# Optimization experiments

Hardware: AMD Instinct MI355X
Metric: run time of the kernel (lower is better)

## Reference

```python
import math
import jax, jax.numpy as jnp
import numpy as np

B, C, H, W = 2, 256, 128, 128
C8 = C // 8
MAX_TOKENS = 4096
S = int(math.isqrt(MAX_TOKENS))  # 64; H,W divisible by S -> exact 2x2 mean pool


def setup_inputs() -> dict:
    key = jax.random.key(0)
    ks = jax.random.split(key, 8)
    sc = 1.0 / math.sqrt(C)
    return {
        "x": jax.random.normal(ks[0], (B, C, H, W), dtype=jnp.float32),
        "Wq": jax.random.normal(ks[1], (C8, C), dtype=jnp.float32) * sc,
        "bq": jax.random.normal(ks[2], (C8,), dtype=jnp.float32) * 0.01,
        "Wk": jax.random.normal(ks[3], (C8, C), dtype=jnp.float32) * sc,
        "bk": jax.random.normal(ks[4], (C8,), dtype=jnp.float32) * 0.01,
        "Wv": jax.random.normal(ks[5], (C, C), dtype=jnp.float32) * sc,
        "bv": jax.random.normal(ks[6], (C,), dtype=jnp.float32) * 0.01,
        # torch inits gamma to 0; use small nonzero so the attention path is exercised
        "gamma": jax.random.normal(ks[7], (1,), dtype=jnp.float32) * 0.1,
    }


def _pool_to_s(t):
    # adaptive_avg_pool2d to (S,S); exact since H%S==0, W%S==0
    b, ch, h, w = t.shape
    return t.reshape(b, ch, S, h // S, S, w // S).mean(axis=(3, 5))


def reference(x, Wq, bq, Wk, bk, Wv, bv, gamma):
    b, c, h, w = x.shape
    # 1x1 convs as channel contractions
    q = jnp.einsum('bchw,oc->bohw', x, Wq) + bq[None, :, None, None]   # (b,c8,h,w)
    k = jnp.einsum('bchw,oc->bohw', x, Wk) + bk[None, :, None, None]   # (b,c8,h,w)
    v = jnp.einsum('bchw,oc->bohw', x, Wv) + bv[None, :, None, None]   # (b,c,h,w)

    q = q.reshape(b, C8, h * w).transpose(0, 2, 1)                      # (b, hw, c8)
    if h * w > MAX_TOKENS:
        k = _pool_to_s(k)
        v = _pool_to_s(v)
    k = k.reshape(b, C8, -1)                                            # (b, c8, s2)
    v = v.reshape(b, c, -1)                                             # (b, c, s2)

    attn = jnp.einsum('btc,bcs->bts', q, k) / math.sqrt(k.shape[1])     # (b, hw, s2)
    attn = jax.nn.softmax(attn, axis=-1)
    out = jnp.einsum('bcs,bts->bct', v, attn).reshape(b, c, h, w)
    return gamma[0] * out + x
```

## Files before the change

### kernel.cpp

```cpp
#include <hip/hip_runtime.h>

typedef unsigned short u16;
typedef unsigned int u32;
typedef unsigned long long u64;
typedef float f32x4 __attribute__((ext_vector_type(4)));
typedef __bf16 bf16x8 __attribute__((ext_vector_type(8)));

__device__ __forceinline__ u16 f2bf(float f) {
  unsigned u = __float_as_uint(f);
  unsigned r = u + 0x7fffu + ((u >> 16) & 1u);
  return (u16)(r >> 16);
}
__device__ __forceinline__ u32 cvt_pk_bf16(float lo, float hi) {
  u32 r;
  asm("v_cvt_pk_bf16_f32 %0, %1, %2" : "=v"(r) : "v"(lo), "v"(hi));
  return r;
}
__device__ __forceinline__ float exp2_hw(float x) {
  float r;
  asm("v_exp_f32 %0, %1" : "=v"(r) : "v"(x));
  return r;
}
__device__ __forceinline__ bf16x8 f32x8_to_bf16x8(float4 a, float4 b) {
  union { u32 u[4]; bf16x8 v; } t;
  t.u[0] = cvt_pk_bf16(a.x, a.y);
  t.u[1] = cvt_pk_bf16(a.z, a.w);
  t.u[2] = cvt_pk_bf16(b.x, b.y);
  t.u[3] = cvt_pk_bf16(b.z, b.w);
  return t.v;
}
__device__ __forceinline__ void gload_lds16(const void* g, u16* l) {
  __builtin_amdgcn_global_load_lds(
      (const __attribute__((address_space(1))) unsigned int*)g,
      (__attribute__((address_space(3))) unsigned int*)l, 16, 0, 0);
}

#define QSCALE 0.25513936f

__global__ __launch_bounds__(256) void proj_kernel(
    const float* __restrict__ x, const float* __restrict__ Wq, const float* __restrict__ bq,
    const float* __restrict__ Wk, const float* __restrict__ bk, const float* __restrict__ Wv,
    const float* __restrict__ bv, u16* __restrict__ Qb, u16* __restrict__ Kt,
    u16* __restrict__ Vb) {
  __shared__ __align__(16) u16 smem[24576];
  const int tid = threadIdx.x;
  const int lane = tid & 63, w = tid >> 6;
  const int l15 = lane & 15, l4 = lane >> 4;
  const int bi = blockIdx.x;
  const f32x4 zero = {0.f, 0.f, 0.f, 0.f};

  if (bi >= 256) {
    u16* xt = smem;
    u16* wq = smem + 16384;
    const int j = bi - 256;
    const int b = j >> 8, tb = j & 255;
    const float* xp = x + (size_t)b * 256 * 16384 + tb * 64;

    for (int i = tid; i < 4096; i += 256) {
      int oc = i >> 7, c0 = (i & 127) * 2;
      float2 f = *reinterpret_cast<const float2*>(Wq + oc * 256 + c0);
      u32 pk = cvt_pk_bf16(f.x * QSCALE, f.y * QSCALE);
      *reinterpret_cast<u32*>((char*)wq + oc * 512 + (((c0 >> 3) ^ (oc & 7)) * 16) +
                              (c0 & 7) * 2) = pk;
    }
#pragma unroll
    for (int rr = 0; rr < 4; ++rr) {
      int c = rr * 64 + (tid >> 2);
      int tch = (tid & 3) * 16;
      const float* src = xp + (size_t)c * 16384 + tch;
#pragma unroll
      for (int u = 0; u < 4; ++u) {
        float4 f = *reinterpret_cast<const float4*>(src + u * 4);
        int t = tch + u * 4;
        *reinterpret_cast<u16*>((char*)xt + (t + 0) * 512 + (((c >> 3) ^ ((t + 0) & 7)) * 16) + (c & 7) * 2) = f2bf(f.x);
        *reinterpret_cast<u16*>((char*)xt + (t + 1) * 512 + (((c >> 3) ^ ((t + 1) & 7)) * 16) + (c & 7) * 2) = f2bf(f.y);
        *reinterpret_cast<u16*>((char*)xt + (t + 2) * 512 + (((c >> 3) ^ ((t + 2) & 7)) * 16) + (c & 7) * 2) = f2bf(f.z);
        *reinterpret_cast<u16*>((char*)xt + (t + 3) * 512 + (((c >> 3) ^ ((t + 3) & 7)) * 16) + (c & 7) * 2) = f2bf(f.w);
      }
    }
    __syncthreads();

    f32x4 acc[2] = {zero, zero};
    const int tl = w * 16 + l15;
#pragma unroll
    for (int k = 0; k < 8; ++k) {
      bf16x8 bf = *reinterpret_cast<const bf16x8*>((char*)xt + tl * 512 +
                                                   (((k * 4 + l4) ^ (tl & 7)) * 16));
#pragma unroll
      for (int m = 0; m < 2; ++m) {
        int oc = m * 16 + l15;
        bf16x8 af = *reinterpret_cast<const bf16x8*>((char*)wq + oc * 512 +
                                                     (((k * 4 + l4) ^ (oc & 7)) * 16));
        acc[m] = __builtin_amdgcn_mfma_f32_16x16x32_bf16(af, bf, acc[m], 0, 0, 0);
      }
    }
    const int t = tb * 64 + tl;
#pragma unroll
    for (int m = 0; m < 2; ++m) {
      int oc0 = m * 16 + l4 * 4;
      u32 p0 = cvt_pk_bf16(acc[m][0] + bq[oc0] * QSCALE, acc[m][1] + bq[oc0 + 1] * QSCALE);
      u32 p1 = cvt_pk_bf16(acc[m][2] + bq[oc0 + 2] * QSCALE, acc[m][3] + bq[oc0 + 3] * QSCALE);
      u16* dst = Qb + ((size_t)b * 16384 + t) * 32 + oc0;
      *reinterpret_cast<u32*>(dst) = p0;
      *reinterpret_cast<u32*>(dst + 2) = p1;
    }
  } else {
    u16* xs = smem;
    const int b = bi >> 7, r2 = bi & 127;
    const int sy = r2 >> 1, z = r2 & 1;
    const int mb = z * 8;
    const float* xb = x + (size_t)b * 256 * 16384;

#pragma unroll
    for (int rr = 0; rr < 4; ++rr) {
      int c = rr * 64 + (tid >> 2);
      int f4base = (tid & 3) * 8;
      const float* r0 = xb + (size_t)c * 16384 + (size_t)sy * 256;
#pragma unroll
      for (int u = 0; u < 8; ++u) {
        int jj = f4base + u;
        float4 a = *reinterpret_cast<const float4*>(r0 + jj * 4);
        float4 d = *reinterpret_cast<const float4*>(r0 + 128 + jj * 4);
        float p0 = (a.x + a.y + d.x + d.y) * 0.25f;
        float p1 = (a.z + a.w + d.z + d.w) * 0.25f;
        int s0 = jj * 2;
        *reinterpret_cast<u16*>((char*)xs + (s0 + 0) * 512 + (((c >> 3) ^ ((s0 + 0) & 7)) * 16) + (c & 7) * 2) = f2bf(p0);
        *reinterpret_cast<u16*>((char*)xs + (s0 + 1) * 512 + (((c >> 3) ^ ((s0 + 1) & 7)) * 16) + (c & 7) * 2) = f2bf(p1);
      }
    }
    __syncthreads();

    f32x4 acc[10];
#pragma unroll
    for (int m = 0; m < 10; ++m) acc[m] = zero;
    const int sl = w * 16 + l15;
#pragma unroll
    for (int k = 0; k < 8; ++k) {
      bf16x8 bf = *reinterpret_cast<const bf16x8*>((char*)xs + sl * 512 +
                                                   (((k * 4 + l4) ^ (sl & 7)) * 16));
      if (z == 0) {
#pragma unroll
        for (int m = 0; m < 2; ++m) {
          const float* wr = Wk + (size_t)(m * 16 + l15) * 256 + k * 32 + l4 * 8;
          float4 fa = *reinterpret_cast<const float4*>(wr);
          float4 fb = *reinterpret_cast<const float4*>(wr + 4);
          acc[m] = __builtin_amdgcn_mfma_f32_16x16x32_bf16(f32x8_to_bf16x8(fa, fb), bf, acc[m], 0, 0, 0);
        }
      }
#pragma unroll
      for (int mm = 0; mm < 8; ++mm) {
        const float* wr = Wv + (size_t)((mb + mm) * 16 + l15) * 256 + k * 32 + l4 * 8;
        float4 fa = *reinterpret_cast<const float4*>(wr);
        float4 fb = *reinterpret_cast<const float4*>(wr + 4);
        acc[2 + mm] = __builtin_amdgcn_mfma_f32_16x16x32_bf16(f32x8_to_bf16x8(fa, fb), bf, acc[2 + mm], 0, 0, 0);
      }
    }
    if (z == 0) {
#pragma unroll
      for (int m = 0; m < 2; ++m) {
        int oc0 = m * 16 + l4 * 4;
        u32 p0 = cvt_pk_bf16(acc[m][0] + bk[oc0], acc[m][1] + bk[oc0 + 1]);
        u32 p1 = cvt_pk_bf16(acc[m][2] + bk[oc0 + 2], acc[m][3] + bk[oc0 + 3]);
        u16* dst = Kt + ((size_t)b * 4096 + sy * 64 + sl) * 32 + oc0;
        *reinterpret_cast<u32*>(dst) = p0;
        *reinterpret_cast<u32*>(dst + 2) = p1;
      }
    }
#pragma unroll
    for (int mm = 0; mm < 8; ++mm) {
#pragma unroll
      for (int r = 0; r < 4; ++r) {
        int oc = (mb + mm) * 16 + l4 * 4 + r;
        Vb[((size_t)b * 256 + oc) * 4096 + sy * 64 + sl] = f2bf(acc[2 + mm][r] + bv[oc]);
      }
    }
  }
}

__global__ __launch_bounds__(256, 2) void attn_kernel(
    const u16* __restrict__ Qb, const u16* __restrict__ Kt, const u16* __restrict__ Vb,
    const float* __restrict__ x, const float* __restrict__ gamma, float* __restrict__ out) {
  __shared__ __align__(16) u16 p_lds[2][64 * 64];
  __shared__ __align__(16) u16 v_lds[2][256 * 64];

  const int tid = threadIdx.x;
  const int lane = tid & 63, w = tid >> 6;
  const int l15 = lane & 15, l4 = lane >> 4, l7 = l15 & 7;
  const int raw = blockIdx.x;
  const int xcd = raw & 7, loc = raw >> 3;
  const int b = xcd >> 2;
  const int tt = (xcd & 3) * 64 + loc;
  const int t0 = tt * 64;

  const u16* Qp = Qb + (size_t)(b * 16384 + t0) * 32;
  const char* Kpc = (const char*)(Kt + (size_t)b * 4096 * 32);
  const char* Vpc = (const char*)(Vb + (size_t)b * 256 * 4096);

  bf16x8 qfr[4];
#pragma unroll
  for (int mt = 0; mt < 4; ++mt)
    qfr[mt] = *reinterpret_cast<const bf16x8*>(Qp + (size_t)(mt * 16 + l15) * 32 + l4 * 8);

  const int key = w * 16 + l15;
  const int pw_chunk = w * 2 + (l4 >> 1), pw_off = (l4 & 1) * 8;

  char* pA0 = (char*)p_lds + l15 * 128 + ((l4 ^ l7) * 16);
  char* pA1 = (char*)p_lds + l15 * 128 + (((4 ^ l4) ^ l7) * 16);
  char* pW = (char*)p_lds + l15 * 128 + ((pw_chunk ^ l7) * 16) + pw_off;
  char* pV0 = (char*)v_lds + (w * 64 + l15) * 128 + ((l4 ^ l7) * 16);
  char* pV1 = (char*)v_lds + (w * 64 + l15) * 128 + (((4 ^ l4) ^ l7) * 16);

  const int sch = lane >> 3;
  const int skc = (lane & 7) ^ sch;
  const u32 vstg0 = (u32)(w * 64 + sch) * 8192 + (u32)skc * 16;
  u32 vstg = vstg0 + 128;
  u32 vok = 2 * 4096 + (u32)key * 64 + (u32)l4 * 16;

  f32x4 acc[4][4] = {};
  float lsum[4] = {};
  const f32x4 zero = {0.f, 0.f, 0.f, 0.f};

#pragma unroll
  for (int i = 0; i < 8; ++i)
    gload_lds16(Vpc + vstg0 + i * 65536, (u16*)v_lds + (w * 8 + i) * 512);
  {
    bf16x8 k0 = *reinterpret_cast<const bf16x8*>(Kpc + ((size_t)key * 64 + l4 * 16));
#pragma unroll
    for (int mt = 0; mt < 4; ++mt) {
      f32x4 s = __builtin_amdgcn_mfma_f32_16x16x32_bf16(k0, qfr[mt], zero, 0, 0, 0);
      float p0 = exp2_hw(fminf(s[0], 28.f)), p1 = exp2_hw(fminf(s[1], 28.f));
      float p2 = exp2_hw(fminf(s[2], 28.f)), p3 = exp2_hw(fminf(s[3], 28.f));
      lsum[mt] += (p0 + p1) + (p2 + p3);
      *reinterpret_cast<u64*>(pW + mt * 2048) =
          (u64)cvt_pk_bf16(p0, p1) | ((u64)cvt_pk_bf16(p2, p3) << 32);
    }
  }
  bf16x8 kfrA = *reinterpret_cast<const bf16x8*>(Kpc + (4096 + (size_t)key * 64 + l4 * 16));
  bf16x8 kfrB;
  __syncthreads();

#define ATTN_ITER(KT, CUR, KC, KN)                                                        \
  {                                                                                       \
                    \
    if ((KT) < 63) {                                                                      \
      _Pragma("unroll") for (int i = 0; i < 8; ++i)                                       \
          gload_lds16(Vpc + vstg + i * 65536,                                             \
                      (u16*)v_lds + (((CUR) ^ 1) * 16384) + (w * 8 + i) * 512);           \
      vstg += 128;                                                                        \
    }                                                                                     \
                              \
    bf16x8 afr0[4], vfr0[4];                                                              \
    _Pragma("unroll") for (int mt = 0; mt < 4; ++mt)                                      \
        afr0[mt] = *reinterpret_cast<const bf16x8*>(pA0 + ((CUR)*8192 + mt * 2048));      \
    _Pragma("unroll") for (int nt = 0; nt < 4; ++nt)                                      \
        vfr0[nt] = *reinterpret_cast<const bf16x8*>(pV0 + ((CUR)*32768 + nt * 2048));     \
                    \
    if ((KT) < 63) {                                                                      \
      _Pragma("unroll") for (int mt = 0; mt < 4; ++mt) {                                  \
        f32x4 s = __builtin_amdgcn_mfma_f32_16x16x32_bf16(KC, qfr[mt], zero, 0, 0, 0);    \
        float p0 = exp2_hw(fminf(s[0], 28.f)), p1 = exp2_hw(fminf(s[1], 28.f));           \
        float p2 = exp2_hw(fminf(s[2], 28.f)), p3 = exp2_hw(fminf(s[3], 28.f));           \
        lsum[mt] += (p0 + p1) + (p2 + p3);                                                \
        *reinterpret_cast<u64*>(pW + (((CUR) ^ 1) * 8192 + mt * 2048)) =                  \
            (u64)cvt_pk_bf16(p0, p1) | ((u64)cvt_pk_bf16(p2, p3) << 32);                  \
      }                                                                                   \
      if ((KT) < 62) { KN = *reinterpret_cast<const bf16x8*>(Kpc + vok); vok += 4096; }   \
    }                                                                                     \
                                                  \
    __builtin_amdgcn_s_setprio(1);                                                        \
    _Pragma("unroll") for (int mt = 0; mt < 4; ++mt)                                      \
      _Pragma("unroll") for (int nt = 0; nt < 4; ++nt)                                    \
        acc[mt][nt] =                                                                     \
            __builtin_amdgcn_mfma_f32_16x16x32_bf16(afr0[mt], vfr0[nt], acc[mt][nt], 0, 0, 0); \
    bf16x8 afr1[4], vfr1[4];                                                              \
    _Pragma("unroll") for (int mt = 0; mt < 4; ++mt)                                      \
        afr1[mt] = *reinterpret_cast<const bf16x8*>(pA1 + ((CUR)*8192 + mt * 2048));      \
    _Pragma("unroll") for (int nt = 0; nt < 4; ++nt)                                      \
        vfr1[nt] = *reinterpret_cast<const bf16x8*>(pV1 + ((CUR)*32768 + nt * 2048));     \
    _Pragma("unroll") for (int mt = 0; mt < 4; ++mt)                                      \
      _Pragma("unroll") for (int nt = 0; nt < 4; ++nt)                                    \
        acc[mt][nt] =                                                                     \
            __builtin_amdgcn_mfma_f32_16x16x32_bf16(afr1[mt], vfr1[nt], acc[mt][nt], 0, 0, 0); \
    __builtin_amdgcn_s_setprio(0);                                                        \
    __syncthreads();                                                                      \
  }

  for (int it = 0; it < 32; ++it) {
    ATTN_ITER(2 * it, 0, kfrA, kfrB)
    ATTN_ITER(2 * it + 1, 1, kfrB, kfrA)
  }
#undef ATTN_ITER

  float* lred = (float*)v_lds;
#pragma unroll
  for (int mt = 0; mt < 4; ++mt) {
    lsum[mt] += __shfl_xor(lsum[mt], 16, 64);
    lsum[mt] += __shfl_xor(lsum[mt], 32, 64);
  }
  if (l4 == 0) {
#pragma unroll
    for (int mt = 0; mt < 4; ++mt) lred[w * 64 + mt * 16 + l15] = lsum[mt];
  }
  __syncthreads();

  const float g = gamma[0];
  float linv[16];
#pragma unroll
  for (int mt = 0; mt < 4; ++mt)
#pragma unroll
    for (int r = 0; r < 4; ++r) {
      int tok = mt * 16 + l4 * 4 + r;
      linv[mt * 4 + r] =
          1.0f / (lred[tok] + lred[64 + tok] + lred[128 + tok] + lred[192 + tok]);
    }
#pragma unroll
  for (int mt = 0; mt < 4; ++mt) {
#pragma unroll
    for (int nt = 0; nt < 4; ++nt) {
      int ch = w * 64 + nt * 16 + l15;
      size_t idx = ((size_t)(b * 256 + ch)) * 16384 + t0 + mt * 16 + l4 * 4;
      float4 xr = *reinterpret_cast<const float4*>(x + idx);
      float4 o;
      o.x = g * acc[mt][nt][0] * linv[mt * 4 + 0] + xr.x;
      o.y = g * acc[mt][nt][1] * linv[mt * 4 + 1] + xr.y;
      o.z = g * acc[mt][nt][2] * linv[mt * 4 + 2] + xr.z;
      o.w = g * acc[mt][nt][3] * linv[mt * 4 + 3] + xr.w;
      *reinterpret_cast<float4*>(out + idx) = o;
    }
  }
}

extern "C" void kernel_launch(void* const* d_in, const int* in_sizes, int n_in,
                              void* d_out, int out_size, void* d_ws, size_t ws_size,
                              hipStream_t stream) {
  const float* x = (const float*)d_in[0];
  const float* Wq = (const float*)d_in[1];
  const float* bq = (const float*)d_in[2];
  const float* Wk = (const float*)d_in[3];
  const float* bk = (const float*)d_in[4];
  const float* Wv = (const float*)d_in[5];
  const float* bv = (const float*)d_in[6];
  const float* gamma = (const float*)d_in[7];
  float* out = (float*)d_out;

  char* ws = (char*)d_ws;
  u16* Qb = (u16*)ws;
  u16* Kt = (u16*)(ws + (2u << 20));
  u16* Vb = (u16*)(ws + (2u << 20) + (512u << 10));

  proj_kernel<<<dim3(768), 256, 0, stream>>>(x, Wq, bq, Wk, bk, Wv, bv, Qb, Kt, Vb);
  attn_kernel<<<dim3(512), 256, 0, stream>>>(Qb, Kt, Vb, x, gamma, out);
}
```

Before: 126.6 us.

## Fuse Q projection into attention kernel, drop Q workspace round-trip

```diff
diff --git a/kernel.cpp b/kernel.cpp
--- a/kernel.cpp
+++ b/kernel.cpp
@@ -37,30 +37,117 @@
 
 #define QSCALE 0.25513936f
 
-__global__ __launch_bounds__(256) void proj_kernel(
-    const float* __restrict__ x, const float* __restrict__ Wq, const float* __restrict__ bq,
-    const float* __restrict__ Wk, const float* __restrict__ bk, const float* __restrict__ Wv,
-    const float* __restrict__ bv, u16* __restrict__ Qb, u16* __restrict__ Kt,
+__global__ __launch_bounds__(256) void proj_kv(
+    const float* __restrict__ x, const float* __restrict__ Wk, const float* __restrict__ bk,
+    const float* __restrict__ Wv, const float* __restrict__ bv, u16* __restrict__ Kt,
     u16* __restrict__ Vb) {
-  __shared__ __align__(16) u16 smem[24576];
+  __shared__ __align__(16) u16 xs[16384];
   const int tid = threadIdx.x;
   const int lane = tid & 63, w = tid >> 6;
   const int l15 = lane & 15, l4 = lane >> 4;
   const int bi = blockIdx.x;
+  const int b = bi >> 7, r2 = bi & 127;
+  const int sy = r2 >> 1, z = r2 & 1;
+  const int mb = z * 8;
+  const float* xb = x + (size_t)b * 256 * 16384;
   const f32x4 zero = {0.f, 0.f, 0.f, 0.f};
 
-  if (bi >= 256) {
-    u16* xt = smem;
-    u16* wq = smem + 16384;
-    const int j = bi - 256;
-    const int b = j >> 8, tb = j & 255;
-    const float* xp = x + (size_t)b * 256 * 16384 + tb * 64;
+#pragma unroll
+  for (int rr = 0; rr < 4; ++rr) {
+    int c = rr * 64 + (tid >> 2);
+    int f4base = (tid & 3) * 8;
+    const float* r0 = xb + (size_t)c * 16384 + (size_t)sy * 256;
+#pragma unroll
+    for (int u = 0; u < 8; ++u) {
+      int jj = f4base + u;
+      float4 a = *reinterpret_cast<const float4*>(r0 + jj * 4);
+      float4 d = *reinterpret_cast<const float4*>(r0 + 128 + jj * 4);
+      float p0 = (a.x + a.y + d.x + d.y) * 0.25f;
+      float p1 = (a.z + a.w + d.z + d.w) * 0.25f;
+      int s0 = jj * 2;
+      *reinterpret_cast<u16*>((char*)xs + (s0 + 0) * 512 + (((c >> 3) ^ ((s0 + 0) & 7)) * 16) + (c & 7) * 2) = f2bf(p0);
+      *reinterpret_cast<u16*>((char*)xs + (s0 + 1) * 512 + (((c >> 3) ^ ((s0 + 1) & 7)) * 16) + (c & 7) * 2) = f2bf(p1);
+    }
+  }
+  __syncthreads();
+
+  f32x4 acc[10];
+#pragma unroll
+  for (int m = 0; m < 10; ++m) acc[m] = zero;
+  const int sl = w * 16 + l15;
+#pragma unroll
+  for (int k = 0; k < 8; ++k) {
+    bf16x8 bf = *reinterpret_cast<const bf16x8*>((char*)xs + sl * 512 +
+                                                 (((k * 4 + l4) ^ (sl & 7)) * 16));
+    if (z == 0) {
+#pragma unroll
+      for (int m = 0; m < 2; ++m) {
+        const float* wr = Wk + (size_t)(m * 16 + l15) * 256 + k * 32 + l4 * 8;
+        float4 fa = *reinterpret_cast<const float4*>(wr);
+        float4 fb = *reinterpret_cast<const float4*>(wr + 4);
+        acc[m] = __builtin_amdgcn_mfma_f32_16x16x32_bf16(f32x8_to_bf16x8(fa, fb), bf, acc[m], 0, 0, 0);
+      }
+    }
+#pragma unroll
+    for (int mm = 0; mm < 8; ++mm) {
+      const float* wr = Wv + (size_t)((mb + mm) * 16 + l15) * 256 + k * 32 + l4 * 8;
+      float4 fa = *reinterpret_cast<const float4*>(wr);
+      float4 fb = *reinterpret_cast<const float4*>(wr + 4);
+      acc[2 + mm] = __builtin_amdgcn_mfma_f32_16x16x32_bf16(f32x8_to_bf16x8(fa, fb), bf, acc[2 + mm], 0, 0, 0);
+    }
+  }
+  if (z == 0) {
+#pragma unroll
+    for (int m = 0; m < 2; ++m) {
+      int oc0 = m * 16 + l4 * 4;
+      u32 p0 = cvt_pk_bf16(acc[m][0] + bk[oc0], acc[m][1] + bk[oc0 + 1]);
+      u32 p1 = cvt_pk_bf16(acc[m][2] + bk[oc0 + 2], acc[m][3] + bk[oc0 + 3]);
+      u16* dst = Kt + ((size_t)b * 4096 + sy * 64 + sl) * 32 + oc0;
+      *reinterpret_cast<u32*>(dst) = p0;
+      *reinterpret_cast<u32*>(dst + 2) = p1;
+    }
+  }
+#pragma unroll
+  for (int mm = 0; mm < 8; ++mm) {
+#pragma unroll
+    for (int r = 0; r < 4; ++r) {
+      int oc = (mb + mm) * 16 + l4 * 4 + r;
+      Vb[((size_t)b * 256 + oc) * 4096 + sy * 64 + sl] = f2bf(acc[2 + mm][r] + bv[oc]);
+    }
+  }
+}
+
+__global__ __launch_bounds__(256, 2) void attn_kernel(
+    const float* __restrict__ x, const float* __restrict__ Wq, const float* __restrict__ bq,
+    const u16* __restrict__ Kt, const u16* __restrict__ Vb, const float* __restrict__ gamma,
+    float* __restrict__ out) {
+  __shared__ __align__(16) u16 p_lds[2][64 * 64];
+  __shared__ __align__(16) u16 v_lds[2][256 * 64];
+
+  const int tid = threadIdx.x;
+  const int lane = tid & 63, w = tid >> 6;
+  const int l15 = lane & 15, l4 = lane >> 4, l7 = l15 & 7;
+  const int raw = blockIdx.x;
+  const int xcd = raw & 7, loc = raw >> 3;
+  const int b = xcd >> 2;
+  const int tt = (xcd & 3) * 64 + loc;
+  const int t0 = tt * 64;
+  const f32x4 zero = {0.f, 0.f, 0.f, 0.f};
+
+  const char* Kpc = (const char*)(Kt + (size_t)b * 4096 * 32);
+  const char* Vpc = (const char*)(Vb + (size_t)b * 256 * 4096);
+
+  {
+    u16* xt = (u16*)v_lds;
+    u16* wqs = (u16*)v_lds + 16384;
+    u16* qlds = (u16*)p_lds + 4096;
+    const float* xp = x + (size_t)b * 256 * 16384 + t0;
 
     for (int i = tid; i < 4096; i += 256) {
       int oc = i >> 7, c0 = (i & 127) * 2;
       float2 f = *reinterpret_cast<const float2*>(Wq + oc * 256 + c0);
       u32 pk = cvt_pk_bf16(f.x * QSCALE, f.y * QSCALE);
-      *reinterpret_cast<u32*>((char*)wq + oc * 512 + (((c0 >> 3) ^ (oc & 7)) * 16) +
+      *reinterpret_cast<u32*>((char*)wqs + oc * 512 + (((c0 >> 3) ^ (oc & 7)) * 16) +
                               (c0 & 7) * 2) = pk;
     }
 #pragma unroll
@@ -80,126 +167,37 @@
     }
     __syncthreads();
 
-    f32x4 acc[2] = {zero, zero};
+    f32x4 qacc[2] = {zero, zero};
     const int tl = w * 16 + l15;
 #pragma unroll
     for (int k = 0; k < 8; ++k) {
-      bf16x8 bf = *reinterpret_cast<const bf16x8*>((char*)xt + tl * 512 +
-                                                   (((k * 4 + l4) ^ (tl & 7)) * 16));
+      bf16x8 bfx = *reinterpret_cast<const bf16x8*>((char*)xt + tl * 512 +
+                                                    (((k * 4 + l4) ^ (tl & 7)) * 16));
 #pragma unroll
       for (int m = 0; m < 2; ++m) {
         int oc = m * 16 + l15;
-        bf16x8 af = *reinterpret_cast<const bf16x8*>((char*)wq + oc * 512 +
+        bf16x8 af = *reinterpret_cast<const bf16x8*>((char*)wqs + oc * 512 +
                                                      (((k * 4 + l4) ^ (oc & 7)) * 16));
-        acc[m] = __builtin_amdgcn_mfma_f32_16x16x32_bf16(af, bf, acc[m], 0, 0, 0);
+        qacc[m] = __builtin_amdgcn_mfma_f32_16x16x32_bf16(af, bfx, qacc[m], 0, 0, 0);
       }
     }
-    const int t = tb * 64 + tl;
 #pragma unroll
     for (int m = 0; m < 2; ++m) {
       int oc0 = m * 16 + l4 * 4;
-      u32 p0 = cvt_pk_bf16(acc[m][0] + bq[oc0] * QSCALE, acc[m][1] + bq[oc0 + 1] * QSCALE);
-      u32 p1 = cvt_pk_bf16(acc[m][2] + bq[oc0 + 2] * QSCALE, acc[m][3] + bq[oc0 + 3] * QSCALE);
-      u16* dst = Qb + ((size_t)b * 16384 + t) * 32 + oc0;
+      u32 p0 = cvt_pk_bf16(qacc[m][0] + bq[oc0] * QSCALE, qacc[m][1] + bq[oc0 + 1] * QSCALE);
+      u32 p1 = cvt_pk_bf16(qacc[m][2] + bq[oc0 + 2] * QSCALE, qacc[m][3] + bq[oc0 + 3] * QSCALE);
+      u16* dst = qlds + tl * 32 + oc0;
       *reinterpret_cast<u32*>(dst) = p0;
       *reinterpret_cast<u32*>(dst + 2) = p1;
     }
-  } else {
-    u16* xs = smem;
-    const int b = bi >> 7, r2 = bi & 127;
-    const int sy = r2 >> 1, z = r2 & 1;
-    const int mb = z * 8;
-    const float* xb = x + (size_t)b * 256 * 16384;
-
-#pragma unroll
-    for (int rr = 0; rr < 4; ++rr) {
-      int c = rr * 64 + (tid >> 2);
-      int f4base = (tid & 3) * 8;
-      const float* r0 = xb + (size_t)c * 16384 + (size_t)sy * 256;
-#pragma unroll
-      for (int u = 0; u < 8; ++u) {
-        int jj = f4base + u;
-        float4 a = *reinterpret_cast<const float4*>(r0 + jj * 4);
-        float4 d = *reinterpret_cast<const float4*>(r0 + 128 + jj * 4);
-        float p0 = (a.x + a.y + d.x + d.y) * 0.25f;
-        float p1 = (a.z + a.w + d.z + d.w) * 0.25f;
-        int s0 = jj * 2;
-        *reinterpret_cast<u16*>((char*)xs + (s0 + 0) * 512 + (((c >> 3) ^ ((s0 + 0) & 7)) * 16) + (c & 7) * 2) = f2bf(p0);
-        *reinterpret_cast<u16*>((char*)xs + (s0 + 1) * 512 + (((c >> 3) ^ ((s0 + 1) & 7)) * 16) + (c & 7) * 2) = f2bf(p1);
-      }
-    }
-    __syncthreads();
-
-    f32x4 acc[10];
-#pragma unroll
-    for (int m = 0; m < 10; ++m) acc[m] = zero;
-    const int sl = w * 16 + l15;
-#pragma unroll
-    for (int k = 0; k < 8; ++k) {
-      bf16x8 bf = *reinterpret_cast<const bf16x8*>((char*)xs + sl * 512 +
-                                                   (((k * 4 + l4) ^ (sl & 7)) * 16));
-      if (z == 0) {
-#pragma unroll
-        for (int m = 0; m < 2; ++m) {
-          const float* wr = Wk + (size_t)(m * 16 + l15) * 256 + k * 32 + l4 * 8;
-          float4 fa = *reinterpret_cast<const float4*>(wr);
-          float4 fb = *reinterpret_cast<const float4*>(wr + 4);
-          acc[m] = __builtin_amdgcn_mfma_f32_16x16x32_bf16(f32x8_to_bf16x8(fa, fb), bf, acc[m], 0, 0, 0);
-        }
-      }
-#pragma unroll
-      for (int mm = 0; mm < 8; ++mm) {
-        const float* wr = Wv + (size_t)((mb + mm) * 16 + l15) * 256 + k * 32 + l4 * 8;
-        float4 fa = *reinterpret_cast<const float4*>(wr);
-        float4 fb = *reinterpret_cast<const float4*>(wr + 4);
-        acc[2 + mm] = __builtin_amdgcn_mfma_f32_16x16x32_bf16(f32x8_to_bf16x8(fa, fb), bf, acc[2 + mm], 0, 0, 0);
-      }
-    }
-    if (z == 0) {
-#pragma unroll
-      for (int m = 0; m < 2; ++m) {
-        int oc0 = m * 16 + l4 * 4;
-        u32 p0 = cvt_pk_bf16(acc[m][0] + bk[oc0], acc[m][1] + bk[oc0 + 1]);
-        u32 p1 = cvt_pk_bf16(acc[m][2] + bk[oc0 + 2], acc[m][3] + bk[oc0 + 3]);
-        u16* dst = Kt + ((size_t)b * 4096 + sy * 64 + sl) * 32 + oc0;
-        *reinterpret_cast<u32*>(dst) = p0;
-        *reinterpret_cast<u32*>(dst + 2) = p1;
-      }
-    }
-#pragma unroll
-    for (int mm = 0; mm < 8; ++mm) {
-#pragma unroll
-      for (int r = 0; r < 4; ++r) {
-        int oc = (mb + mm) * 16 + l4 * 4 + r;
-        Vb[((size_t)b * 256 + oc) * 4096 + sy * 64 + sl] = f2bf(acc[2 + mm][r] + bv[oc]);
-      }
-    }
-  }
-}
-
-__global__ __launch_bounds__(256, 2) void attn_kernel(
-    const u16* __restrict__ Qb, const u16* __restrict__ Kt, const u16* __restrict__ Vb,
-    const float* __restrict__ x, const float* __restrict__ gamma, float* __restrict__ out) {
-  __shared__ __align__(16) u16 p_lds[2][64 * 64];
-  __shared__ __align__(16) u16 v_lds[2][256 * 64];
-
-  const int tid = threadIdx.x;
-  const int lane = tid & 63, w = tid >> 6;
-  const int l15 = lane & 15, l4 = lane >> 4, l7 = l15 & 7;
-  const int raw = blockIdx.x;
-  const int xcd = raw & 7, loc = raw >> 3;
-  const int b = xcd >> 2;
-  const int tt = (xcd & 3) * 64 + loc;
-  const int t0 = tt * 64;
-
-  const u16* Qp = Qb + (size_t)(b * 16384 + t0) * 32;
-  const char* Kpc = (const char*)(Kt + (size_t)b * 4096 * 32);
-  const char* Vpc = (const char*)(Vb + (size_t)b * 256 * 4096);
+  }
+  __syncthreads();
 
   bf16x8 qfr[4];
 #pragma unroll
   for (int mt = 0; mt < 4; ++mt)
-    qfr[mt] = *reinterpret_cast<const bf16x8*>(Qp + (size_t)(mt * 16 + l15) * 32 + l4 * 8);
+    qfr[mt] = *reinterpret_cast<const bf16x8*>((u16*)p_lds + 4096 +
+                                               (mt * 16 + l15) * 32 + l4 * 8);
 
   const int key = w * 16 + l15;
   const int pw_chunk = w * 2 + (l4 >> 1), pw_off = (l4 & 1) * 8;
@@ -218,7 +216,6 @@
 
   f32x4 acc[4][4] = {};
   float lsum[4] = {};
-  const f32x4 zero = {0.f, 0.f, 0.f, 0.f};
 
 #pragma unroll
   for (int i = 0; i < 8; ++i)
@@ -254,7 +251,7 @@
         afr0[mt] = *reinterpret_cast<const bf16x8*>(pA0 + ((CUR)*8192 + mt * 2048));      \
     _Pragma("unroll") for (int nt = 0; nt < 4; ++nt)                                      \
         vfr0[nt] = *reinterpret_cast<const bf16x8*>(pV0 + ((CUR)*32768 + nt * 2048));     \
-                    \
+                                \
     if ((KT) < 63) {                                                                      \
       _Pragma("unroll") for (int mt = 0; mt < 4; ++mt) {                                  \
         f32x4 s = __builtin_amdgcn_mfma_f32_16x16x32_bf16(KC, qfr[mt], zero, 0, 0, 0);    \
@@ -344,10 +341,9 @@
   float* out = (float*)d_out;
 
   char* ws = (char*)d_ws;
-  u16* Qb = (u16*)ws;
-  u16* Kt = (u16*)(ws + (2u << 20));
-  u16* Vb = (u16*)(ws + (2u << 20) + (512u << 10));
-
-  proj_kernel<<<dim3(768), 256, 0, stream>>>(x, Wq, bq, Wk, bk, Wv, bv, Qb, Kt, Vb);
-  attn_kernel<<<dim3(512), 256, 0, stream>>>(Qb, Kt, Vb, x, gamma, out);
-}
+  u16* Kt = (u16*)ws;
+  u16* Vb = (u16*)(ws + (512u << 10));
+
+  proj_kv<<<dim3(256), 256, 0, stream>>>(x, Wk, bk, Wv, bv, Kt, Vb);
+  attn_kernel<<<dim3(512), 256, 0, stream>>>(x, Wq, bq, Kt, Vb, gamma, out);
+}
```

After: 147.0 us. 1.16x slower.
